# Kernel optimization log

Measured on AMD Instinct MI355X. Metric: run time of the kernel, lower is better.

## Reference

```python
import jax, jax.numpy as jnp
import numpy as np

L, B, S, E, N = 4, 1, 2048, 768, 12
H = E // N
FF = 4 * E
EPS = 1e-5


def setup_inputs() -> dict:
    key = jax.random.key(0)
    ks = jax.random.split(key, 12)
    g = lambda i, shape, sc=0.02: jax.random.normal(ks[i], shape, jnp.float32) * sc
    return {
        "x": jax.random.normal(ks[0], (B, S, E), jnp.float32),
        "mask": jnp.tril(jnp.ones((1, 1, S, S), jnp.int32)),  # causal
        "c_attn_w": g(1, (L, E, 3 * E)),
        "c_attn_b": g(2, (L, 3 * E)),
        "c_proj_w": g(3, (L, E, E)),
        "c_proj_b": g(4, (L, E)),
        "ln1_w": jnp.ones((L, E), jnp.float32),
        "ln1_b": jnp.zeros((L, E), jnp.float32),
        "fc_w": g(5, (L, E, FF)),
        "fc_b": g(6, (L, FF)),
        "proj_w": g(7, (L, FF, E)),
        "proj_b": g(8, (L, E)),
        "ln2_w": jnp.ones((L, E), jnp.float32),
        "ln2_b": jnp.zeros((L, E), jnp.float32),
        "lnf_w": jnp.ones((E,), jnp.float32),
        "lnf_b": jnp.zeros((E,), jnp.float32),
    }


def _layer_norm(x, w, b):
    m = jnp.mean(x, axis=-1, keepdims=True)
    v = jnp.mean(jnp.square(x - m), axis=-1, keepdims=True)
    return (x - m) * jax.lax.rsqrt(v + EPS) * w + b


def reference(x, mask, c_attn_w, c_attn_b, c_proj_w, c_proj_b,
              ln1_w, ln1_b, fc_w, fc_b, proj_w, proj_b,
              ln2_w, ln2_b, lnf_w, lnf_b):
    masked = (mask == 0)  # [1,1,S,S] bool, True where attention is disallowed
    # cf_ composes right-to-left: Decoder applies final LayerNorm FIRST,
    # then blocks in reversed list order (scan reverse=True), dropout=identity (eval).
    h0 = _layer_norm(x, lnf_w, lnf_b)

    def block(h, p):
        Wqkv, bqkv, Wp, bp, w1, b1, Wf, bf, Wo, bo, w2, b2 = p
        qkv = h @ Wqkv + bqkv                      # [B,S,3E]
        q, k, v = jnp.split(qkv, 3, axis=-1)
        hd = lambda t: t.reshape(B, S, N, H).transpose(0, 2, 1, 3)  # [B,N,S,H]
        q, k, v = hd(q), hd(k), hd(v)
        att = jnp.einsum('bnsh,bnth->bnst', q, k) / jnp.sqrt(jnp.float32(H))
        att = jnp.where(masked, -jnp.inf, att)
        att = jax.nn.softmax(att, axis=-1)         # [B,N,S,S]
        y = jnp.einsum('bnst,bnth->bnsh', att, v)  # [B,N,S,H]
        y = y.transpose(0, 2, 1, 3).reshape(B, S, E) @ Wp + bp
        h = _layer_norm(y + h, w1, b1)             # post-norm residual 1
        m = jax.nn.gelu(h @ Wf + bf, approximate=False) @ Wo + bo
        h = _layer_norm(m + h, w2, b2)             # post-norm residual 2
        return h, None

    out, _ = jax.lax.scan(
        block, h0,
        (c_attn_w, c_attn_b, c_proj_w, c_proj_b, ln1_w, ln1_b,
         fc_w, fc_b, proj_w, proj_b, ln2_w, ln2_b),
        reverse=True)
    return out
```

## Files before the change

### kernel.cpp

```cpp
#include <hip/hip_runtime.h>
#include <hip/hip_bf16.h>
#include <math.h>

#define S_LEN 2048
#define E_DIM 768
#define NHEAD 12
#define FF_DIM 3072
#define L_LAYERS 4

typedef __attribute__((ext_vector_type(8))) short short8;
typedef __attribute__((ext_vector_type(4))) float f32x4;
typedef __attribute__((ext_vector_type(4))) unsigned short ushort4_t;
typedef __attribute__((ext_vector_type(2))) unsigned int uint2v;

__device__ __forceinline__ unsigned short f2bf(float f) {
  union { float f; unsigned u; } v; v.f = f;
  unsigned r = v.u + 0x7fffu + ((v.u >> 16) & 1u);
  return (unsigned short)(r >> 16);
}

__device__ __forceinline__ unsigned cvtpk(float lo, float hi) {
  unsigned r;
  asm("v_cvt_pk_bf16_f32 %0, %1, %2" : "=v"(r) : "v"(lo), "v"(hi));
  return r;
}

__device__ __forceinline__ f32x4 MFMA(short8 a, short8 b, f32x4 c) {
  return __builtin_amdgcn_mfma_f32_16x16x32_bf16(a, b, c, 0, 0, 0);
}

__device__ __forceinline__ void gld_lds16(const void* g, void* l) {
  __builtin_amdgcn_global_load_lds(
      (const __attribute__((address_space(1))) void*)g,
      (__attribute__((address_space(3))) void*)l, 16, 0, 0);
}

__global__ __launch_bounds__(256)
void transpose_cast(const float* __restrict__ src, short* __restrict__ dst,
                    int K, int Nn) {
  __shared__ float tile[32][33];
  src += (size_t)blockIdx.z * K * Nn;
  dst += (size_t)blockIdx.z * K * Nn;
  const int i0 = blockIdx.x * 32;
  const int j0 = blockIdx.y * 32;
  const int tx = threadIdx.x & 31, ty = threadIdx.x >> 5;
#pragma unroll
  for (int r = 0; r < 32; r += 8)
    tile[ty + r][tx] = src[(size_t)(i0 + ty + r) * Nn + j0 + tx];
  __syncthreads();
#pragma unroll
  for (int r = 0; r < 32; r += 8)
    dst[(size_t)(j0 + ty + r) * K + i0 + tx] = (short)f2bf(tile[tx][ty + r]);
}

__global__ __launch_bounds__(256)
void ln_kernel(const float* __restrict__ parts, int P,
               const float* __restrict__ b2, const float* __restrict__ colBias,
               const float* __restrict__ w, const float* __restrict__ bb,
               float* __restrict__ outF, short* __restrict__ outB) {
  const int row = blockIdx.x;
  const int t = threadIdx.x;
  __shared__ float red[4], red2[4];
  float v[3];
  const size_t plane = (size_t)S_LEN * E_DIM;
#pragma unroll
  for (int i = 0; i < 3; ++i) {
    const int c = t + i * 256;
    float acc = colBias ? colBias[c] : 0.f;
    if (b2) acc += b2[(size_t)row * E_DIM + c];
    for (int p = 0; p < P; ++p)
      acc += parts[p * plane + (size_t)row * E_DIM + c];
    v[i] = acc;
  }
  float s = v[0] + v[1] + v[2];
#pragma unroll
  for (int off = 32; off; off >>= 1) s += __shfl_down(s, off);
  const int ln = t & 63, wv = t >> 6;
  if (ln == 0) red[wv] = s;
  __syncthreads();
  const float mean = (red[0] + red[1] + red[2] + red[3]) * (1.0f / E_DIM);
  float qs = 0.f;
#pragma unroll
  for (int i = 0; i < 3; ++i) { float d = v[i] - mean; qs += d * d; }
#pragma unroll
  for (int off = 32; off; off >>= 1) qs += __shfl_down(qs, off);
  if (ln == 0) red2[wv] = qs;
  __syncthreads();
  const float var = (red2[0] + red2[1] + red2[2] + red2[3]) * (1.0f / E_DIM);
  const float rs = rsqrtf(var + 1e-5f);
#pragma unroll
  for (int i = 0; i < 3; ++i) {
    const int c = t + i * 256;
    float o = (v[i] - mean) * rs * w[c] + bb[c];
    outF[(size_t)row * E_DIM + c] = o;
    outB[(size_t)row * E_DIM + c] = (short)f2bf(o);
  }
}

template <int EPI>
__global__ __launch_bounds__(512)
void gemm_nt(const short* __restrict__ A, const short* __restrict__ Bt,
             const float* __restrict__ bias, float* __restrict__ outF,
             short* __restrict__ outB, short* __restrict__ qOut,
             short* __restrict__ kOut, short* __restrict__ vtOut,
             int M, int Nn, int K, int kLen) {
  __shared__ alignas(16) short As[2][64 * 64];
  __shared__ alignas(16) short Bs[2][128 * 64];
  const int bm = blockIdx.x, bn = blockIdx.y;
  const int t = threadIdx.x;
  const int ln = t & 63, wv = t >> 6;
  const int wr = wv >> 2, wcn = wv & 3;
  const int lr = ln & 15, lg = ln >> 4;
  const int l7 = lr & 7;
  f32x4 acc[2][2] = {};

  const int kStart = blockIdx.z * kLen;
  const int nSteps = kLen / 64;
  const int srow = ln >> 3;
  const int sg = (ln & 7) ^ srow;
  const short* aSrc = A + (size_t)bm * 64 * K + (size_t)(wv * 8 + srow) * K +
                      kStart + sg * 8;
  const short* bSrc0 = Bt + (size_t)bn * 128 * K + (size_t)(wv * 8 + srow) * K +
                       kStart + sg * 8;
  const short* bSrc1 = bSrc0 + (size_t)64 * K;

  auto stage = [&](int buf, int ko) {
    gld_lds16(aSrc + ko, &As[buf][wv * 512]);
    gld_lds16(bSrc0 + ko, &Bs[buf][wv * 512]);
    gld_lds16(bSrc1 + ko, &Bs[buf][(wv + 8) * 512]);
  };

  stage(0, 0);
  __syncthreads();
  int cur = 0;
  for (int s = 0; s < nSteps; ++s) {
    if (s + 1 < nSteps) stage(cur ^ 1, (s + 1) * 64);
    short8 af[2][2], bfr[2][2];
#pragma unroll
    for (int m = 0; m < 2; ++m)
#pragma unroll
      for (int kk = 0; kk < 2; ++kk)
        af[m][kk] = *(const short8*)(&As[cur][(wr * 32 + m * 16 + lr) * 64 +
                                             (((kk * 4 + lg) ^ l7) * 8)]);
#pragma unroll
    for (int n = 0; n < 2; ++n)
#pragma unroll
      for (int kk = 0; kk < 2; ++kk)
        bfr[n][kk] = *(const short8*)(&Bs[cur][(wcn * 32 + n * 16 + lr) * 64 +
                                              (((kk * 4 + lg) ^ l7) * 8)]);
#pragma unroll
    for (int m = 0; m < 2; ++m)
#pragma unroll
      for (int n = 0; n < 2; ++n)
#pragma unroll
        for (int kk = 0; kk < 2; ++kk)
          acc[m][n] = MFMA(af[m][kk], bfr[n][kk], acc[m][n]);
    __syncthreads();
    cur ^= 1;
  }

  if constexpr (EPI == 0) outF += (size_t)blockIdx.z * ((size_t)M * Nn);

#pragma unroll
  for (int m = 0; m < 2; ++m) {
#pragma unroll
    for (int n = 0; n < 2; ++n) {
      const int colb = bn * 128 + wcn * 32 + n * 16;
      const int row0 = bm * 64 + wr * 32 + m * 16 + lg * 4;
      if constexpr (EPI == 0) {
#pragma unroll
        for (int r = 0; r < 4; ++r)
          outF[(size_t)(row0 + r) * Nn + colb + lr] = acc[m][n][r];
      } else if constexpr (EPI == 1) {
#pragma unroll
        for (int r = 0; r < 4; ++r) {
          float vv = acc[m][n][r] + bias[colb + lr];
          float g = 0.5f * vv * (1.0f + erff(vv * 0.70710678118f));
          outB[(size_t)(row0 + r) * Nn + colb + lr] = (short)f2bf(g);
        }
      } else {
        float vv[4];
#pragma unroll
        for (int r = 0; r < 4; ++r) vv[r] = acc[m][n][r] + bias[colb + lr];
        const int which = colb / E_DIM;
        const int wcolb = colb - which * E_DIM;
        const int head = wcolb >> 6;
        const int hh = (wcolb & 63) + lr;
        if (which == 2) {
          ushort4_t pk;
#pragma unroll
          for (int r = 0; r < 4; ++r) pk[r] = f2bf(vv[r]);
          *(ushort4_t*)(vtOut + ((size_t)head * 64 + hh) * S_LEN + row0) = pk;
        } else if (which == 0) {
#pragma unroll
          for (int r = 0; r < 4; ++r)
            qOut[((size_t)head * S_LEN + row0 + r) * 64 + hh] =
                (short)f2bf(vv[r] * 0.125f);
        } else {
#pragma unroll
          for (int r = 0; r < 4; ++r)
            kOut[((size_t)head * S_LEN + row0 + r) * 64 + hh] =
                (short)f2bf(vv[r]);
        }
      }
    }
  }
}

__global__ __launch_bounds__(256)
void attn_kernel(const short* __restrict__ q, const short* __restrict__ k,
                 const short* __restrict__ vt, short* __restrict__ y,
                 float* __restrict__ pO, float* __restrict__ pL) {
  __shared__ alignas(16) short KS[2][64 * 64];
  __shared__ alignas(16) short VS[2][64 * 64];
  __shared__ alignas(16) short P[4][16 * 64];
  const int bx = blockIdx.x;
  int head, qt, tile0, ntl, mode;
  bool hasDiag;
  if (bx < 192) {
    head = bx % NHEAD; qt = 31 - bx / NHEAD;
    tile0 = 0; ntl = 16; hasDiag = false; mode = 1;
  } else if (bx < 384) {
    const int b = bx - 192;
    head = b % NHEAD; qt = 31 - b / NHEAD;
    tile0 = 16; ntl = qt + 1 - 16; hasDiag = true; mode = 2;
  } else {
    const int b = bx - 384;
    head = b % NHEAD; qt = 15 - b / NHEAD;
    tile0 = 0; ntl = qt + 1; hasDiag = true; mode = 0;
  }
  const int qb = qt * 64;
  const int t = threadIdx.x;
  const int ln = t & 63, wv = t >> 6;
  const int lr = ln & 15, lg = ln >> 4;
  const int l7 = lr & 7;

  const int srow = ln >> 3;
  const int sg = (ln & 7) ^ srow;
  const short* kbase = k + (size_t)head * S_LEN * 64;
  const short* vbase = vt + (size_t)head * 64 * S_LEN;

  auto stage = [&](int buf, int t0) {
#pragma unroll
    for (int i = 0; i < 2; ++i) {
      const int c = wv * 2 + i;
      gld_lds16(kbase + (size_t)(t0 + c * 8 + srow) * 64 + sg * 8,
                &KS[buf][c * 512]);
      gld_lds16(vbase + (size_t)(c * 8 + srow) * S_LEN + t0 + sg * 8,
                &VS[buf][c * 512]);
    }
  };

  short8 qa[2];
  {
    const short* qp =
        q + ((size_t)head * S_LEN + qb + wv * 16 + lr) * 64 + lg * 8;
    qa[0] = *(const short8*)qp;
    qa[1] = *(const short8*)(qp + 32);
  }

  f32x4 o[4] = {};
  float lrun = 0.f;

  stage(0, tile0 * 64);
  for (int i = 0; i < ntl; ++i) {
    __syncthreads();
    if (i + 1 < ntl) stage((i + 1) & 1, (tile0 + i + 1) * 64);
    const short* KSb = KS[i & 1];
    const short* VSb = VS[i & 1];
    const int t0 = (tile0 + i) * 64;

    f32x4 sc[4];
#pragma unroll
    for (int cc = 0; cc < 4; ++cc) {
      f32x4 z = {};
#pragma unroll
      for (int kk = 0; kk < 2; ++kk)
        z = MFMA(*(const short8*)(KSb + (cc * 16 + lr) * 64 +
                                  (((kk * 4 + lg) ^ l7) * 8)),
                 qa[kk], z);
      sc[cc] = z;
    }

    if (hasDiag && i == ntl - 1) {
      const int qg = qb + wv * 16 + lr;
#pragma unroll
      for (int cc = 0; cc < 4; ++cc)
#pragma unroll
        for (int r = 0; r < 4; ++r)
          if (t0 + cc * 16 + lg * 4 + r > qg) sc[cc][r] = -1e30f;
    }

    float ss = 0.f;
    unsigned pk[8];
#pragma unroll
    for (int cc = 0; cc < 4; ++cc) {
      const float p0 = __expf(sc[cc][0]);
      const float p1 = __expf(sc[cc][1]);
      const float p2 = __expf(sc[cc][2]);
      const float p3 = __expf(sc[cc][3]);
      ss += (p0 + p1) + (p2 + p3);
      pk[2 * cc] = cvtpk(p0, p1);
      pk[2 * cc + 1] = cvtpk(p2, p3);
    }
    ss += __shfl_xor(ss, 16);
    ss += __shfl_xor(ss, 32);
    lrun += ss;

#pragma unroll
    for (int cc = 0; cc < 4; ++cc) {
      uint2v w2; w2.x = pk[2 * cc]; w2.y = pk[2 * cc + 1];
      *(uint2v*)(&P[wv][lr * 64 + (((cc * 2 + (lg >> 1)) ^ l7) * 8) +
                        (lg & 1) * 4]) = w2;
    }

    short8 pa[2];
#pragma unroll
    for (int kk = 0; kk < 2; ++kk)
      pa[kk] = *(const short8*)(&P[wv][lr * 64 + (((kk * 4 + lg) ^ l7) * 8)]);
#pragma unroll
    for (int n = 0; n < 4; ++n)
#pragma unroll
      for (int kk = 0; kk < 2; ++kk)
        o[n] = MFMA(pa[kk],
                    *(const short8*)(VSb + (n * 16 + lr) * 64 +
                                     (((kk * 4 + lg) ^ l7) * 8)),
                    o[n]);
  }

  if (mode == 0) {
    float inv[4];
#pragma unroll
    for (int r = 0; r < 4; ++r) inv[r] = 1.0f / __shfl(lrun, lg * 4 + r);
#pragma unroll
    for (int n = 0; n < 4; ++n)
#pragma unroll
      for (int r = 0; r < 4; ++r)
        y[(size_t)(qb + wv * 16 + lg * 4 + r) * E_DIM + head * 64 + n * 16 +
          lr] = (short)f2bf(o[n][r] * inv[r]);
  } else {
    const int p = (qt - 16) * NHEAD + head;
    float* ob = pO + ((size_t)(mode - 1) * 192 + p) * 4096;
#pragma unroll
    for (int n = 0; n < 4; ++n)
#pragma unroll
      for (int r = 0; r < 4; ++r)
        ob[(wv * 16 + lg * 4 + r) * 64 + n * 16 + lr] = o[n][r];
    float* lb = pL + ((size_t)(mode - 1) * 192 + p) * 64;
    if (lg == 0) lb[wv * 16 + lr] = lrun;
  }
}

__global__ __launch_bounds__(256)
void attn_merge(const float* __restrict__ pO, const float* __restrict__ pL,
                short* __restrict__ y) {
  const int p = blockIdx.x;
  const int qt = 16 + p / NHEAD, head = p % NHEAD;
  const int t = threadIdx.x;
  const int hd = t & 63, q0 = t >> 6;
  const float* o1 = pO + (size_t)p * 4096;
  const float* o2 = pO + (size_t)(192 + p) * 4096;
  const float* l1 = pL + (size_t)p * 64;
  const float* l2 = pL + (size_t)(192 + p) * 64;
#pragma unroll
  for (int i = 0; i < 16; ++i) {
    const int qq = q0 + i * 4;
    const float inv = 1.0f / (l1[qq] + l2[qq]);
    const float val = (o1[qq * 64 + hd] + o2[qq * 64 + hd]) * inv;
    y[(size_t)(qt * 64 + qq) * E_DIM + head * 64 + hd] = (short)f2bf(val);
  }
}

extern "C" void kernel_launch(void* const* d_in, const int* in_sizes, int n_in,
                              void* d_out, int out_size, void* d_ws,
                              size_t ws_size, hipStream_t stream) {
  const float* x       = (const float*)d_in[0];
  const float* attn_w  = (const float*)d_in[2];
  const float* attn_b  = (const float*)d_in[3];
  const float* cproj_w = (const float*)d_in[4];
  const float* cproj_b = (const float*)d_in[5];
  const float* ln1_w   = (const float*)d_in[6];
  const float* ln1_b   = (const float*)d_in[7];
  const float* fc_w    = (const float*)d_in[8];
  const float* fc_b    = (const float*)d_in[9];
  const float* proj_w  = (const float*)d_in[10];
  const float* proj_b  = (const float*)d_in[11];
  const float* ln2_w   = (const float*)d_in[12];
  const float* ln2_b   = (const float*)d_in[13];
  const float* lnf_w   = (const float*)d_in[14];
  const float* lnf_b   = (const float*)d_in[15];

  char* ws = (char*)d_ws;
  size_t off = 0;
  auto alloc = [&](size_t bytes) {
    char* p = ws + off;
    off += (bytes + 255) & ~(size_t)255;
    return p;
  };
  short* attnT = (short*)alloc((size_t)L_LAYERS * E_DIM * 3 * E_DIM * 2);
  short* projT = (short*)alloc((size_t)L_LAYERS * E_DIM * E_DIM * 2);
  short* fcT   = (short*)alloc((size_t)L_LAYERS * E_DIM * FF_DIM * 2);
  short* p2T   = (short*)alloc((size_t)L_LAYERS * FF_DIM * E_DIM * 2);
  float* hF    = (float*)alloc((size_t)S_LEN * E_DIM * 4);
  short* hB    = (short*)alloc((size_t)S_LEN * E_DIM * 2);
  short* qB    = (short*)alloc((size_t)NHEAD * S_LEN * 64 * 2);
  short* kB    = (short*)alloc((size_t)NHEAD * S_LEN * 64 * 2);
  short* vT    = (short*)alloc((size_t)NHEAD * S_LEN * 64 * 2);
  short* yB    = (short*)alloc((size_t)S_LEN * E_DIM * 2);
  short* aB    = (short*)alloc((size_t)S_LEN * FF_DIM * 2);
  float* partF = (float*)alloc((size_t)4 * S_LEN * E_DIM * 4);
  float* pO = partF;
  float* pL = partF + 2 * 192 * 4096;

  transpose_cast<<<dim3(E_DIM / 32, 3 * E_DIM / 32, L_LAYERS), 256, 0, stream>>>(
      attn_w, attnT, E_DIM, 3 * E_DIM);
  transpose_cast<<<dim3(E_DIM / 32, E_DIM / 32, L_LAYERS), 256, 0, stream>>>(
      cproj_w, projT, E_DIM, E_DIM);
  transpose_cast<<<dim3(E_DIM / 32, FF_DIM / 32, L_LAYERS), 256, 0, stream>>>(
      fc_w, fcT, E_DIM, FF_DIM);
  transpose_cast<<<dim3(FF_DIM / 32, E_DIM / 32, L_LAYERS), 256, 0, stream>>>(
      proj_w, p2T, FF_DIM, E_DIM);

  ln_kernel<<<S_LEN, 256, 0, stream>>>(x, 1, nullptr, nullptr, lnf_w, lnf_b,
                                       hF, hB);

  for (int l = L_LAYERS - 1; l >= 0; --l) {
    gemm_nt<2><<<dim3(S_LEN / 64, 3 * E_DIM / 128, 1), 512, 0, stream>>>(
        hB, attnT + (size_t)l * E_DIM * 3 * E_DIM,
        attn_b + (size_t)l * 3 * E_DIM, nullptr, nullptr, qB, kB, vT,
        S_LEN, 3 * E_DIM, E_DIM, E_DIM);
    attn_kernel<<<dim3(576), 256, 0, stream>>>(qB, kB, vT, yB, pO, pL);
    attn_merge<<<dim3(192), 256, 0, stream>>>(pO, pL, yB);
    gemm_nt<0><<<dim3(S_LEN / 64, E_DIM / 128, 3), 512, 0, stream>>>(
        yB, projT + (size_t)l * E_DIM * E_DIM, nullptr,
        partF, nullptr, nullptr, nullptr, nullptr, S_LEN, E_DIM, E_DIM, 256);
    ln_kernel<<<S_LEN, 256, 0, stream>>>(partF, 3, hF,
                                         cproj_b + (size_t)l * E_DIM,
                                         ln1_w + (size_t)l * E_DIM,
                                         ln1_b + (size_t)l * E_DIM, hF, hB);
    gemm_nt<1><<<dim3(S_LEN / 64, FF_DIM / 128, 1), 512, 0, stream>>>(
        hB, fcT + (size_t)l * E_DIM * FF_DIM, fc_b + (size_t)l * FF_DIM,
        nullptr, aB, nullptr, nullptr, nullptr, S_LEN, FF_DIM, E_DIM, E_DIM);
    gemm_nt<0><<<dim3(S_LEN / 64, E_DIM / 128, 4), 512, 0, stream>>>(
        aB, p2T + (size_t)l * FF_DIM * E_DIM, nullptr,
        partF, nullptr, nullptr, nullptr, nullptr, S_LEN, E_DIM, FF_DIM, 768);
    float* outTarget = (l == 0) ? (float*)d_out : hF;
    ln_kernel<<<S_LEN, 256, 0, stream>>>(partF, 4, hF,
                                         proj_b + (size_t)l * E_DIM,
                                         ln2_w + (size_t)l * E_DIM,
                                         ln2_b + (size_t)l * E_DIM, outTarget,
                                         hB);
  }
}
```

Measured before the change: 451.5 us.

## Widen attention query tile to 128 rows to reuse K/V tiles across two query groups

Each attention block now handles 128 query rows, with each wave owning two 16-row groups. K and V fragments are loaded from LDS once and used by both groups, which halves K/V staging traffic per query row and halves the block count. The split of long causal rows into two partial halves is remapped to the new 128-row tiles, and the merge kernel is updated to match. The cost is more registers and LDS per block, fewer blocks (288) on a large GPU, and coarser load balance.

```diff
diff --git a/kernel.cpp b/kernel.cpp
--- a/kernel.cpp
+++ b/kernel.cpp
@@ -213,23 +213,23 @@
                  float* __restrict__ pO, float* __restrict__ pL) {
   __shared__ alignas(16) short KS[2][64 * 64];
   __shared__ alignas(16) short VS[2][64 * 64];
-  __shared__ alignas(16) short P[4][16 * 64];
+  __shared__ alignas(16) short P[4][2][16 * 64];
   const int bx = blockIdx.x;
-  int head, qt, tile0, ntl, mode;
+  int head, qj, tile0, ntl, mode;
   bool hasDiag;
-  if (bx < 192) {
-    head = bx % NHEAD; qt = 31 - bx / NHEAD;
-    tile0 = 0; ntl = 16; hasDiag = false; mode = 1;
-  } else if (bx < 384) {
+  if (bx < 96) {
+    head = bx % NHEAD; qj = 15 - bx / NHEAD;
+    tile0 = 0; ntl = qj + 1; hasDiag = false; mode = 1;
+  } else if (bx < 192) {
+    const int b = bx - 96;
+    head = b % NHEAD; qj = 15 - b / NHEAD;
+    tile0 = qj + 1; ntl = qj + 1; hasDiag = true; mode = 2;
+  } else {
     const int b = bx - 192;
-    head = b % NHEAD; qt = 31 - b / NHEAD;
-    tile0 = 16; ntl = qt + 1 - 16; hasDiag = true; mode = 2;
-  } else {
-    const int b = bx - 384;
-    head = b % NHEAD; qt = 15 - b / NHEAD;
-    tile0 = 0; ntl = qt + 1; hasDiag = true; mode = 0;
-  }
-  const int qb = qt * 64;
+    head = b % NHEAD; qj = 7 - b / NHEAD;
+    tile0 = 0; ntl = 2 * qj + 2; hasDiag = true; mode = 0;
+  }
+  const int qb = qj * 128;
   const int t = threadIdx.x;
   const int ln = t & 63, wv = t >> 6;
   const int lr = ln & 15, lg = ln >> 4;
@@ -251,16 +251,17 @@
     }
   };
 
-  short8 qa[2];
-  {
+  short8 qa[2][2];
+#pragma unroll
+  for (int qg = 0; qg < 2; ++qg) {
     const short* qp =
-        q + ((size_t)head * S_LEN + qb + wv * 16 + lr) * 64 + lg * 8;
-    qa[0] = *(const short8*)qp;
-    qa[1] = *(const short8*)(qp + 32);
-  }
-
-  f32x4 o[4] = {};
-  float lrun = 0.f;
+        q + ((size_t)head * S_LEN + qb + wv * 32 + qg * 16 + lr) * 64 + lg * 8;
+    qa[qg][0] = *(const short8*)qp;
+    qa[qg][1] = *(const short8*)(qp + 32);
+  }
+
+  f32x4 o[2][4] = {};
+  float lrun[2] = {0.f, 0.f};
 
   stage(0, tile0 * 64);
   for (int i = 0; i < ntl; ++i) {
@@ -270,84 +271,111 @@
     const short* VSb = VS[i & 1];
     const int t0 = (tile0 + i) * 64;
 
-    f32x4 sc[4];
-#pragma unroll
-    for (int cc = 0; cc < 4; ++cc) {
-      f32x4 z = {};
+    short8 kf[4][2];
+#pragma unroll
+    for (int cc = 0; cc < 4; ++cc)
 #pragma unroll
       for (int kk = 0; kk < 2; ++kk)
-        z = MFMA(*(const short8*)(KSb + (cc * 16 + lr) * 64 +
-                                  (((kk * 4 + lg) ^ l7) * 8)),
-                 qa[kk], z);
-      sc[cc] = z;
-    }
-
-    if (hasDiag && i == ntl - 1) {
-      const int qg = qb + wv * 16 + lr;
-#pragma unroll
-      for (int cc = 0; cc < 4; ++cc)
+        kf[cc][kk] = *(const short8*)(KSb + (cc * 16 + lr) * 64 +
+                                      (((kk * 4 + lg) ^ l7) * 8));
+
+    f32x4 sc[2][4];
+#pragma unroll
+    for (int qg = 0; qg < 2; ++qg)
+#pragma unroll
+      for (int cc = 0; cc < 4; ++cc) {
+        f32x4 z = {};
+#pragma unroll
+        for (int kk = 0; kk < 2; ++kk) z = MFMA(kf[cc][kk], qa[qg][kk], z);
+        sc[qg][cc] = z;
+      }
+
+    if (hasDiag && i >= ntl - 2) {
+#pragma unroll
+      for (int qg = 0; qg < 2; ++qg) {
+        const int qrow = qb + wv * 32 + qg * 16 + lr;
+#pragma unroll
+        for (int cc = 0; cc < 4; ++cc)
+#pragma unroll
+          for (int r = 0; r < 4; ++r)
+            if (t0 + cc * 16 + lg * 4 + r > qrow) sc[qg][cc][r] = -1e30f;
+      }
+    }
+
+#pragma unroll
+    for (int qg = 0; qg < 2; ++qg) {
+      float ss = 0.f;
+      unsigned pk[8];
+#pragma unroll
+      for (int cc = 0; cc < 4; ++cc) {
+        const float p0 = __expf(sc[qg][cc][0]);
+        const float p1 = __expf(sc[qg][cc][1]);
+        const float p2 = __expf(sc[qg][cc][2]);
+        const float p3 = __expf(sc[qg][cc][3]);
+        ss += (p0 + p1) + (p2 + p3);
+        pk[2 * cc] = cvtpk(p0, p1);
+        pk[2 * cc + 1] = cvtpk(p2, p3);
+      }
+      ss += __shfl_xor(ss, 16);
+      ss += __shfl_xor(ss, 32);
+      lrun[qg] += ss;
+#pragma unroll
+      for (int cc = 0; cc < 4; ++cc) {
+        uint2v w2; w2.x = pk[2 * cc]; w2.y = pk[2 * cc + 1];
+        *(uint2v*)(&P[wv][qg][lr * 64 + (((cc * 2 + (lg >> 1)) ^ l7) * 8) +
+                            (lg & 1) * 4]) = w2;
+      }
+    }
+
+    short8 vf[4][2];
+#pragma unroll
+    for (int n = 0; n < 4; ++n)
+#pragma unroll
+      for (int kk = 0; kk < 2; ++kk)
+        vf[n][kk] = *(const short8*)(VSb + (n * 16 + lr) * 64 +
+                                     (((kk * 4 + lg) ^ l7) * 8));
+#pragma unroll
+    for (int qg = 0; qg < 2; ++qg) {
+      short8 pa[2];
+#pragma unroll
+      for (int kk = 0; kk < 2; ++kk)
+        pa[kk] =
+            *(const short8*)(&P[wv][qg][lr * 64 + (((kk * 4 + lg) ^ l7) * 8)]);
+#pragma unroll
+      for (int n = 0; n < 4; ++n)
+#pragma unroll
+        for (int kk = 0; kk < 2; ++kk)
+          o[qg][n] = MFMA(pa[kk], vf[n][kk], o[qg][n]);
+    }
+  }
+
+  if (mode == 0) {
+#pragma unroll
+    for (int qg = 0; qg < 2; ++qg) {
+      float inv[4];
+#pragma unroll
+      for (int r = 0; r < 4; ++r) inv[r] = 1.0f / __shfl(lrun[qg], lg * 4 + r);
+#pragma unroll
+      for (int n = 0; n < 4; ++n)
 #pragma unroll
         for (int r = 0; r < 4; ++r)
-          if (t0 + cc * 16 + lg * 4 + r > qg) sc[cc][r] = -1e30f;
-    }
-
-    float ss = 0.f;
-    unsigned pk[8];
-#pragma unroll
-    for (int cc = 0; cc < 4; ++cc) {
-      const float p0 = __expf(sc[cc][0]);
-      const float p1 = __expf(sc[cc][1]);
-      const float p2 = __expf(sc[cc][2]);
-      const float p3 = __expf(sc[cc][3]);
-      ss += (p0 + p1) + (p2 + p3);
-      pk[2 * cc] = cvtpk(p0, p1);
-      pk[2 * cc + 1] = cvtpk(p2, p3);
-    }
-    ss += __shfl_xor(ss, 16);
-    ss += __shfl_xor(ss, 32);
-    lrun += ss;
-
-#pragma unroll
-    for (int cc = 0; cc < 4; ++cc) {
-      uint2v w2; w2.x = pk[2 * cc]; w2.y = pk[2 * cc + 1];
-      *(uint2v*)(&P[wv][lr * 64 + (((cc * 2 + (lg >> 1)) ^ l7) * 8) +
-                        (lg & 1) * 4]) = w2;
-    }
-
-    short8 pa[2];
-#pragma unroll
-    for (int kk = 0; kk < 2; ++kk)
-      pa[kk] = *(const short8*)(&P[wv][lr * 64 + (((kk * 4 + lg) ^ l7) * 8)]);
-#pragma unroll
-    for (int n = 0; n < 4; ++n)
-#pragma unroll
-      for (int kk = 0; kk < 2; ++kk)
-        o[n] = MFMA(pa[kk],
-                    *(const short8*)(VSb + (n * 16 + lr) * 64 +
-                                     (((kk * 4 + lg) ^ l7) * 8)),
-                    o[n]);
-  }
-
-  if (mode == 0) {
-    float inv[4];
-#pragma unroll
-    for (int r = 0; r < 4; ++r) inv[r] = 1.0f / __shfl(lrun, lg * 4 + r);
-#pragma unroll
-    for (int n = 0; n < 4; ++n)
-#pragma unroll
-      for (int r = 0; r < 4; ++r)
-        y[(size_t)(qb + wv * 16 + lg * 4 + r) * E_DIM + head * 64 + n * 16 +
-          lr] = (short)f2bf(o[n][r] * inv[r]);
+          y[(size_t)(qb + wv * 32 + qg * 16 + lg * 4 + r) * E_DIM + head * 64 +
+            n * 16 + lr] = (short)f2bf(o[qg][n][r] * inv[r]);
+    }
   } else {
-    const int p = (qt - 16) * NHEAD + head;
-    float* ob = pO + ((size_t)(mode - 1) * 192 + p) * 4096;
-#pragma unroll
-    for (int n = 0; n < 4; ++n)
-#pragma unroll
-      for (int r = 0; r < 4; ++r)
-        ob[(wv * 16 + lg * 4 + r) * 64 + n * 16 + lr] = o[n][r];
-    float* lb = pL + ((size_t)(mode - 1) * 192 + p) * 64;
-    if (lg == 0) lb[wv * 16 + lr] = lrun;
+    const int p = (qj - 8) * NHEAD + head;
+    float* ob = pO + ((size_t)(mode - 1) * 96 + p) * 8192;
+    float* lb = pL + ((size_t)(mode - 1) * 96 + p) * 128;
+#pragma unroll
+    for (int qg = 0; qg < 2; ++qg) {
+#pragma unroll
+      for (int n = 0; n < 4; ++n)
+#pragma unroll
+        for (int r = 0; r < 4; ++r)
+          ob[(wv * 32 + qg * 16 + lg * 4 + r) * 64 + n * 16 + lr] =
+              o[qg][n][r];
+      if (lg == 0) lb[wv * 32 + qg * 16 + lr] = lrun[qg];
+    }
   }
 }
 
@@ -355,19 +383,19 @@
 void attn_merge(const float* __restrict__ pO, const float* __restrict__ pL,
                 short* __restrict__ y) {
   const int p = blockIdx.x;
-  const int qt = 16 + p / NHEAD, head = p % NHEAD;
+  const int qj = 8 + p / NHEAD, head = p % NHEAD;
   const int t = threadIdx.x;
   const int hd = t & 63, q0 = t >> 6;
-  const float* o1 = pO + (size_t)p * 4096;
-  const float* o2 = pO + (size_t)(192 + p) * 4096;
-  const float* l1 = pL + (size_t)p * 64;
-  const float* l2 = pL + (size_t)(192 + p) * 64;
-#pragma unroll
-  for (int i = 0; i < 16; ++i) {
+  const float* o1 = pO + (size_t)p * 8192;
+  const float* o2 = pO + (size_t)(96 + p) * 8192;
+  const float* l1 = pL + (size_t)p * 128;
+  const float* l2 = pL + (size_t)(96 + p) * 128;
+#pragma unroll
+  for (int i = 0; i < 32; ++i) {
     const int qq = q0 + i * 4;
     const float inv = 1.0f / (l1[qq] + l2[qq]);
     const float val = (o1[qq * 64 + hd] + o2[qq * 64 + hd]) * inv;
-    y[(size_t)(qt * 64 + qq) * E_DIM + head * 64 + hd] = (short)f2bf(val);
+    y[(size_t)(qj * 128 + qq) * E_DIM + head * 64 + hd] = (short)f2bf(val);
   }
 }
 
@@ -410,7 +438,7 @@
   short* aB    = (short*)alloc((size_t)S_LEN * FF_DIM * 2);
   float* partF = (float*)alloc((size_t)4 * S_LEN * E_DIM * 4);
   float* pO = partF;
-  float* pL = partF + 2 * 192 * 4096;
+  float* pL = partF + 2 * 96 * 8192;
 
   transpose_cast<<<dim3(E_DIM / 32, 3 * E_DIM / 32, L_LAYERS), 256, 0, stream>>>(
       attn_w, attnT, E_DIM, 3 * E_DIM);
@@ -429,8 +457,8 @@
         hB, attnT + (size_t)l * E_DIM * 3 * E_DIM,
         attn_b + (size_t)l * 3 * E_DIM, nullptr, nullptr, qB, kB, vT,
         S_LEN, 3 * E_DIM, E_DIM, E_DIM);
-    attn_kernel<<<dim3(576), 256, 0, stream>>>(qB, kB, vT, yB, pO, pL);
-    attn_merge<<<dim3(192), 256, 0, stream>>>(pO, pL, yB);
+    attn_kernel<<<dim3(288), 256, 0, stream>>>(qB, kB, vT, yB, pO, pL);
+    attn_merge<<<dim3(96), 256, 0, stream>>>(pO, pL, yB);
     gemm_nt<0><<<dim3(S_LEN / 64, E_DIM / 128, 3), 512, 0, stream>>>(
         yB, projT + (size_t)l * E_DIM * E_DIM, nullptr,
         partF, nullptr, nullptr, nullptr, nullptr, S_LEN, E_DIM, E_DIM, 256);
```

Result: slower. 481.9 us (+6.7%).

## Rebalance causal attention split-KV chunks and vectorize LayerNorm to one row per wave

Applied to the files above, without the earlier changes.

The attention work split changes from a fixed two-way split for the upper 16 query tiles to a graded 1/2/3-chunk split across query tiles, giving 756 roughly balanced blocks instead of 576 uneven ones. The merge kernel sums a variable number of partial outputs. Separately, LayerNorm now processes one row per wavefront using float4 loads and stores and xor-shuffle reductions, with no shared memory or block barriers. The cost is more partial-result traffic and a more complex merge.

```diff
diff --git a/kernel.cpp b/kernel.cpp
--- a/kernel.cpp
+++ b/kernel.cpp
@@ -58,42 +58,56 @@
                const float* __restrict__ b2, const float* __restrict__ colBias,
                const float* __restrict__ w, const float* __restrict__ bb,
                float* __restrict__ outF, short* __restrict__ outB) {
-  const int row = blockIdx.x;
   const int t = threadIdx.x;
-  __shared__ float red[4], red2[4];
-  float v[3];
+  const int ln = t & 63, wv = t >> 6;
+  const int row = blockIdx.x * 4 + wv;
   const size_t plane = (size_t)S_LEN * E_DIM;
-#pragma unroll
-  for (int i = 0; i < 3; ++i) {
-    const int c = t + i * 256;
-    float acc = colBias ? colBias[c] : 0.f;
-    if (b2) acc += b2[(size_t)row * E_DIM + c];
-    for (int p = 0; p < P; ++p)
-      acc += parts[p * plane + (size_t)row * E_DIM + c];
-    v[i] = acc;
-  }
-  float s = v[0] + v[1] + v[2];
-#pragma unroll
-  for (int off = 32; off; off >>= 1) s += __shfl_down(s, off);
-  const int ln = t & 63, wv = t >> 6;
-  if (ln == 0) red[wv] = s;
-  __syncthreads();
-  const float mean = (red[0] + red[1] + red[2] + red[3]) * (1.0f / E_DIM);
+  float4 v[3];
+#pragma unroll
+  for (int j = 0; j < 3; ++j) {
+    const int c4 = ln + j * 64;
+    float4 acc = colBias ? ((const float4*)colBias)[c4]
+                         : make_float4(0.f, 0.f, 0.f, 0.f);
+    if (b2) {
+      float4 r = ((const float4*)(b2 + (size_t)row * E_DIM))[c4];
+      acc.x += r.x; acc.y += r.y; acc.z += r.z; acc.w += r.w;
+    }
+    for (int p = 0; p < P; ++p) {
+      float4 r = ((const float4*)(parts + p * plane + (size_t)row * E_DIM))[c4];
+      acc.x += r.x; acc.y += r.y; acc.z += r.z; acc.w += r.w;
+    }
+    v[j] = acc;
+  }
+  float s = 0.f;
+#pragma unroll
+  for (int j = 0; j < 3; ++j) s += (v[j].x + v[j].y) + (v[j].z + v[j].w);
+#pragma unroll
+  for (int off = 32; off; off >>= 1) s += __shfl_xor(s, off);
+  const float mean = s * (1.0f / E_DIM);
   float qs = 0.f;
 #pragma unroll
-  for (int i = 0; i < 3; ++i) { float d = v[i] - mean; qs += d * d; }
-#pragma unroll
-  for (int off = 32; off; off >>= 1) qs += __shfl_down(qs, off);
-  if (ln == 0) red2[wv] = qs;
-  __syncthreads();
-  const float var = (red2[0] + red2[1] + red2[2] + red2[3]) * (1.0f / E_DIM);
-  const float rs = rsqrtf(var + 1e-5f);
-#pragma unroll
-  for (int i = 0; i < 3; ++i) {
-    const int c = t + i * 256;
-    float o = (v[i] - mean) * rs * w[c] + bb[c];
-    outF[(size_t)row * E_DIM + c] = o;
-    outB[(size_t)row * E_DIM + c] = (short)f2bf(o);
+  for (int j = 0; j < 3; ++j) {
+    float dx = v[j].x - mean, dy = v[j].y - mean;
+    float dz = v[j].z - mean, dw = v[j].w - mean;
+    qs += (dx * dx + dy * dy) + (dz * dz + dw * dw);
+  }
+#pragma unroll
+  for (int off = 32; off; off >>= 1) qs += __shfl_xor(qs, off);
+  const float rs = rsqrtf(qs * (1.0f / E_DIM) + 1e-5f);
+#pragma unroll
+  for (int j = 0; j < 3; ++j) {
+    const int c4 = ln + j * 64;
+    const float4 w4 = ((const float4*)w)[c4];
+    const float4 b4 = ((const float4*)bb)[c4];
+    float4 o;
+    o.x = (v[j].x - mean) * rs * w4.x + b4.x;
+    o.y = (v[j].y - mean) * rs * w4.y + b4.y;
+    o.z = (v[j].z - mean) * rs * w4.z + b4.z;
+    o.w = (v[j].w - mean) * rs * w4.w + b4.w;
+    ((float4*)(outF + (size_t)row * E_DIM))[c4] = o;
+    ushort4_t pk;
+    pk[0] = f2bf(o.x); pk[1] = f2bf(o.y); pk[2] = f2bf(o.z); pk[3] = f2bf(o.w);
+    *(ushort4_t*)(outB + (size_t)row * E_DIM + c4 * 4) = pk;
   }
 }
 
@@ -215,20 +229,21 @@
   __shared__ alignas(16) short VS[2][64 * 64];
   __shared__ alignas(16) short P[4][16 * 64];
   const int bx = blockIdx.x;
-  int head, qt, tile0, ntl, mode;
-  bool hasDiag;
-  if (bx < 192) {
-    head = bx % NHEAD; qt = 31 - bx / NHEAD;
-    tile0 = 0; ntl = 16; hasDiag = false; mode = 1;
-  } else if (bx < 384) {
-    const int b = bx - 192;
-    head = b % NHEAD; qt = 31 - b / NHEAD;
-    tile0 = 16; ntl = qt + 1 - 16; hasDiag = true; mode = 2;
+  const int head = bx % NHEAD;
+  const int idx = 62 - bx / NHEAD;
+  int qt, nch, ch;
+  if (idx < 11) {
+    qt = idx; nch = 1; ch = 0;
+  } else if (idx < 33) {
+    qt = 11 + (idx - 11) / 2; nch = 2; ch = (idx - 11) & 1;
   } else {
-    const int b = bx - 384;
-    head = b % NHEAD; qt = 15 - b / NHEAD;
-    tile0 = 0; ntl = qt + 1; hasDiag = true; mode = 0;
-  }
+    qt = 22 + (idx - 33) / 3; nch = 3; ch = (idx - 33) % 3;
+  }
+  const int total = qt + 1;
+  const int cbase = total / nch, crem = total % nch;
+  const int tile0 = ch * cbase + (ch < crem ? ch : crem);
+  const int ntl = cbase + (ch < crem ? 1 : 0);
+  const bool hasDiag = (ch == nch - 1);
   const int qb = qt * 64;
   const int t = threadIdx.x;
   const int ln = t & 63, wv = t >> 6;
@@ -328,7 +343,7 @@
                     o[n]);
   }
 
-  if (mode == 0) {
+  if (nch == 1) {
     float inv[4];
 #pragma unroll
     for (int r = 0; r < 4; ++r) inv[r] = 1.0f / __shfl(lrun, lg * 4 + r);
@@ -339,14 +354,14 @@
         y[(size_t)(qb + wv * 16 + lg * 4 + r) * E_DIM + head * 64 + n * 16 +
           lr] = (short)f2bf(o[n][r] * inv[r]);
   } else {
-    const int p = (qt - 16) * NHEAD + head;
-    float* ob = pO + ((size_t)(mode - 1) * 192 + p) * 4096;
+    const int slot = (idx - 11) + 52 * head;
+    float* ob = pO + (size_t)slot * 4096;
 #pragma unroll
     for (int n = 0; n < 4; ++n)
 #pragma unroll
       for (int r = 0; r < 4; ++r)
         ob[(wv * 16 + lg * 4 + r) * 64 + n * 16 + lr] = o[n][r];
-    float* lb = pL + ((size_t)(mode - 1) * 192 + p) * 64;
+    float* lb = pL + (size_t)slot * 64;
     if (lg == 0) lb[wv * 16 + lr] = lrun;
   }
 }
@@ -355,19 +370,22 @@
 void attn_merge(const float* __restrict__ pO, const float* __restrict__ pL,
                 short* __restrict__ y) {
   const int p = blockIdx.x;
-  const int qt = 16 + p / NHEAD, head = p % NHEAD;
+  const int qt = 11 + p / NHEAD, head = p % NHEAD;
+  const int nch = (qt <= 21) ? 2 : 3;
+  const int b = (qt <= 21) ? 11 + 2 * (qt - 11) : 33 + 3 * (qt - 22);
   const int t = threadIdx.x;
   const int hd = t & 63, q0 = t >> 6;
-  const float* o1 = pO + (size_t)p * 4096;
-  const float* o2 = pO + (size_t)(192 + p) * 4096;
-  const float* l1 = pL + (size_t)p * 64;
-  const float* l2 = pL + (size_t)(192 + p) * 64;
 #pragma unroll
   for (int i = 0; i < 16; ++i) {
     const int qq = q0 + i * 4;
-    const float inv = 1.0f / (l1[qq] + l2[qq]);
-    const float val = (o1[qq * 64 + hd] + o2[qq * 64 + hd]) * inv;
-    y[(size_t)(qt * 64 + qq) * E_DIM + head * 64 + hd] = (short)f2bf(val);
+    float osum = 0.f, lsum = 0.f;
+    for (int c = 0; c < nch; ++c) {
+      const int slot = (b + c - 11) + 52 * head;
+      osum += pO[(size_t)slot * 4096 + qq * 64 + hd];
+      lsum += pL[(size_t)slot * 64 + qq];
+    }
+    y[(size_t)(qt * 64 + qq) * E_DIM + head * 64 + hd] =
+        (short)f2bf(osum / lsum);
   }
 }
 
@@ -410,7 +428,7 @@
   short* aB    = (short*)alloc((size_t)S_LEN * FF_DIM * 2);
   float* partF = (float*)alloc((size_t)4 * S_LEN * E_DIM * 4);
   float* pO = partF;
-  float* pL = partF + 2 * 192 * 4096;
+  float* pL = partF + (size_t)52 * 12 * 4096;
 
   transpose_cast<<<dim3(E_DIM / 32, 3 * E_DIM / 32, L_LAYERS), 256, 0, stream>>>(
       attn_w, attnT, E_DIM, 3 * E_DIM);
@@ -421,23 +439,23 @@
   transpose_cast<<<dim3(FF_DIM / 32, E_DIM / 32, L_LAYERS), 256, 0, stream>>>(
       proj_w, p2T, FF_DIM, E_DIM);
 
-  ln_kernel<<<S_LEN, 256, 0, stream>>>(x, 1, nullptr, nullptr, lnf_w, lnf_b,
-                                       hF, hB);
+  ln_kernel<<<S_LEN / 4, 256, 0, stream>>>(x, 1, nullptr, nullptr, lnf_w,
+                                           lnf_b, hF, hB);
 
   for (int l = L_LAYERS - 1; l >= 0; --l) {
     gemm_nt<2><<<dim3(S_LEN / 64, 3 * E_DIM / 128, 1), 512, 0, stream>>>(
         hB, attnT + (size_t)l * E_DIM * 3 * E_DIM,
         attn_b + (size_t)l * 3 * E_DIM, nullptr, nullptr, qB, kB, vT,
         S_LEN, 3 * E_DIM, E_DIM, E_DIM);
-    attn_kernel<<<dim3(576), 256, 0, stream>>>(qB, kB, vT, yB, pO, pL);
-    attn_merge<<<dim3(192), 256, 0, stream>>>(pO, pL, yB);
+    attn_kernel<<<dim3(63 * NHEAD), 256, 0, stream>>>(qB, kB, vT, yB, pO, pL);
+    attn_merge<<<dim3(21 * NHEAD), 256, 0, stream>>>(pO, pL, yB);
     gemm_nt<0><<<dim3(S_LEN / 64, E_DIM / 128, 3), 512, 0, stream>>>(
         yB, projT + (size_t)l * E_DIM * E_DIM, nullptr,
         partF, nullptr, nullptr, nullptr, nullptr, S_LEN, E_DIM, E_DIM, 256);
-    ln_kernel<<<S_LEN, 256, 0, stream>>>(partF, 3, hF,
-                                         cproj_b + (size_t)l * E_DIM,
-                                         ln1_w + (size_t)l * E_DIM,
-                                         ln1_b + (size_t)l * E_DIM, hF, hB);
+    ln_kernel<<<S_LEN / 4, 256, 0, stream>>>(partF, 3, hF,
+                                             cproj_b + (size_t)l * E_DIM,
+                                             ln1_w + (size_t)l * E_DIM,
+                                             ln1_b + (size_t)l * E_DIM, hF, hB);
     gemm_nt<1><<<dim3(S_LEN / 64, FF_DIM / 128, 1), 512, 0, stream>>>(
         hB, fcT + (size_t)l * E_DIM * FF_DIM, fc_b + (size_t)l * FF_DIM,
         nullptr, aB, nullptr, nullptr, nullptr, S_LEN, FF_DIM, E_DIM, E_DIM);
@@ -445,10 +463,10 @@
         aB, p2T + (size_t)l * FF_DIM * E_DIM, nullptr,
         partF, nullptr, nullptr, nullptr, nullptr, S_LEN, E_DIM, FF_DIM, 768);
     float* outTarget = (l == 0) ? (float*)d_out : hF;
-    ln_kernel<<<S_LEN, 256, 0, stream>>>(partF, 4, hF,
-                                         proj_b + (size_t)l * E_DIM,
-                                         ln2_w + (size_t)l * E_DIM,
-                                         ln2_b + (size_t)l * E_DIM, outTarget,
-                                         hB);
-  }
-}
+    ln_kernel<<<S_LEN / 4, 256, 0, stream>>>(partF, 4, hF,
+                                             proj_b + (size_t)l * E_DIM,
+                                             ln2_w + (size_t)l * E_DIM,
+                                             ln2_b + (size_t)l * E_DIM,
+                                             outTarget, hB);
+  }
+}
```

Result: slower. 497.5 us (+10.2%).
